# Performance work log

Hardware: AMD Instinct MI355X
Metric: run time of the kernel (lower is better)

## Reference

```python
import jax, jax.numpy as jnp
import numpy as np

B, S, D, E, H, K = 4, 2048, 1024, 8, 512, 2


def setup_inputs() -> dict:
    key = jax.random.key(0)
    ks = jax.random.split(key, 11)
    sc = 0.02
    return {
        "x": jax.random.normal(ks[0], (B, S, D), dtype=jnp.float32),
        "gate_W": jax.random.normal(ks[1], (D, E), dtype=jnp.float32) * sc,
        "W1": jax.random.normal(ks[2], (E, D, H), dtype=jnp.float32) * sc,
        "b1": jnp.zeros((E, H), dtype=jnp.float32),
        "W2": jax.random.normal(ks[3], (E, H, D), dtype=jnp.float32) * sc,
        "b2": jnp.zeros((E, D), dtype=jnp.float32),
        "Ws1": jax.random.normal(ks[4], (D, H), dtype=jnp.float32) * sc,
        "bs1": jnp.zeros((H,), dtype=jnp.float32),
        "Ws2": jax.random.normal(ks[5], (H, D), dtype=jnp.float32) * sc,
        "bs2": jnp.zeros((D,), dtype=jnp.float32),
        "route_scale": jnp.ones((), dtype=jnp.float32),
    }


def reference(x, gate_W, W1, b1, W2, b2, Ws1, bs1, Ws2, bs2, route_scale):
    # Gating: sigmoid scores scaled by route_scale (score_func='sigmoid')
    scores = jax.nn.sigmoid(x @ gate_W) * route_scale          # (B,S,E)
    topk_scores, topk_idx = jax.lax.top_k(scores, K)           # (B,S,K)
    topk_w = topk_scores / topk_scores.sum(-1, keepdims=True)  # normalized weights
    # Dense combine weights: zero for non-selected experts (same math as
    # the original sparse gather/scatter loop).
    onehot = jax.nn.one_hot(topk_idx, E, dtype=x.dtype)        # (B,S,K,E)
    gate_full = jnp.einsum('bsk,bske->bse', topk_w, onehot)    # (B,S,E)
    # Per-expert MLP applied to all tokens, combined with sparse gate weights.
    h = jax.nn.gelu(jnp.einsum('bsd,edh->bseh', x, W1) + b1, approximate=False)
    y = jnp.einsum('bseh,ehd->bsed', h, W2) + b2               # (B,S,E,D)
    expert_out = jnp.einsum('bse,bsed->bsd', gate_full, y)     # (B,S,D)
    # Shared expert MLP (always active)
    shared = jax.nn.gelu(x @ Ws1 + bs1, approximate=False) @ Ws2 + bs2
    return expert_out + shared
```

## Files before the change

### kernel.cpp

```cpp
#include <hip/hip_runtime.h>
#include <hip/hip_bf16.h>

#define TOKENS 8192
#define D_DIM  1024
#define E_NUM  8
#define H_DIM  512
#define N1     4608
#define CAP    3072
#define ET256  (CAP / 256)
#define EXP_ROWS (E_NUM * CAP)
#define SH_BASE  EXP_ROWS
#define HS_ROWS (EXP_ROWS + TOKENS)

typedef __bf16 bf16_t;
typedef __bf16 bf16x8 __attribute__((ext_vector_type(8)));
typedef __bf16 bf16x4 __attribute__((ext_vector_type(4)));
typedef float  f32x4  __attribute__((ext_vector_type(4)));

__device__ __forceinline__ float gelu_fast(float v) {
  float w = v * v;
  float t = __builtin_fmaf(w, 0.10294307f, 2.30258835f);
  float z = v * t;
  float e = __builtin_amdgcn_exp2f(z);
  float r = __builtin_amdgcn_rcpf(e + 1.0f);
  return v - v * r;
}

__global__ __launch_bounds__(256) void routing_kernel(
    const float* __restrict__ x, const float* __restrict__ gW,
    const float* __restrict__ route_scale, float* __restrict__ gateT,
    int* __restrict__ sel, bf16_t* __restrict__ Xb) {
  int tok  = blockIdx.x * 4 + (threadIdx.x >> 6);
  int lane = threadIdx.x & 63;
  const float* xr = x + (size_t)tok * D_DIM;
  double p[E_NUM];
#pragma unroll
  for (int e = 0; e < E_NUM; ++e) p[e] = 0.0;
  for (int d = lane; d < D_DIM; d += 64) {
    double xv = (double)xr[d];
    const float* g = gW + (size_t)d * E_NUM;
#pragma unroll
    for (int e = 0; e < E_NUM; ++e) p[e] += xv * (double)g[e];
  }
#pragma unroll
  for (int off = 32; off > 0; off >>= 1) {
#pragma unroll
    for (int e = 0; e < E_NUM; ++e) p[e] += __shfl_xor(p[e], off, 64);
  }
  if (lane == 0) {
    double rs = (double)route_scale[0];
    double s[E_NUM];
#pragma unroll
    for (int e = 0; e < E_NUM; ++e) s[e] = rs / (1.0 + exp(-p[e]));
    int i1 = 0;
#pragma unroll
    for (int e = 1; e < E_NUM; ++e) if (s[e] > s[i1]) i1 = e;
    int i2 = (i1 == 0) ? 1 : 0;
#pragma unroll
    for (int e = 0; e < E_NUM; ++e) if (e != i1 && s[e] > s[i2]) i2 = e;
    double inv = 1.0 / (s[i1] + s[i2]);
    float o[E_NUM];
#pragma unroll
    for (int e = 0; e < E_NUM; ++e) o[e] = 0.f;
    o[i1] = (float)(s[i1] * inv);
    o[i2] = (float)(s[i2] * inv);
#pragma unroll
    for (int e = 0; e < E_NUM; ++e) gateT[(size_t)e * TOKENS + tok] = o[e];
    sel[tok] = i1 * 8 + i2;
  }
  const float4* x4 = (const float4*)xr;
  bf16x4* xb4 = (bf16x4*)(Xb + (size_t)tok * D_DIM);
#pragma unroll
  for (int i = 0; i < 4; ++i) {
    float4 v = x4[i * 64 + lane];
    bf16x4 o = { (bf16_t)v.x, (bf16_t)v.y, (bf16_t)v.z, (bf16_t)v.w };
    xb4[i * 64 + lane] = o;
  }
}

__global__ __launch_bounds__(256) void repack1_kernel(
    const float* __restrict__ W1, const float* __restrict__ Ws1,
    bf16_t* __restrict__ Bt1) {
  __shared__ float tile[32][33];
  int k0 = blockIdx.x * 32, n0 = blockIdx.y * 32;
  int tx = threadIdx.x, ty = threadIdx.y;
#pragma unroll
  for (int i = 0; i < 4; ++i) {
    int kl = ty + i * 8;
    int n = n0 + tx, k = k0 + kl;
    float v;
    if (n0 < 4096) v = W1[(size_t)(n >> 9) * (D_DIM * H_DIM) + (size_t)k * H_DIM + (n & 511)];
    else           v = Ws1[(size_t)k * H_DIM + (n - 4096)];
    tile[kl][tx] = v;
  }
  __syncthreads();
#pragma unroll
  for (int i = 0; i < 4; ++i) {
    int nl = ty + i * 8;
    Bt1[(size_t)(n0 + nl) * D_DIM + k0 + tx] = (bf16_t)tile[tx][nl];
  }
}

__global__ __launch_bounds__(256) void repack2e_kernel(
    const float* __restrict__ W2, const float* __restrict__ Ws2,
    bf16_t* __restrict__ Bt2e) {
  __shared__ float tile[32][33];
  int d0 = blockIdx.x * 32, h0 = blockIdx.y * 32, e = blockIdx.z;
  int tx = threadIdx.x, ty = threadIdx.y;
#pragma unroll
  for (int i = 0; i < 4; ++i) {
    int hl = ty + i * 8;
    int h = h0 + hl, d = d0 + tx;
    float v = (e < E_NUM) ? W2[((size_t)e * H_DIM + h) * D_DIM + d]
                          : Ws2[(size_t)h * D_DIM + d];
    tile[hl][tx] = v;
  }
  __syncthreads();
#pragma unroll
  for (int i = 0; i < 4; ++i) {
    int dl = ty + i * 8;
    Bt2e[((size_t)e * D_DIM + (d0 + dl)) * H_DIM + h0 + tx] = (bf16_t)tile[tx][dl];
  }
}

__global__ __launch_bounds__(256) void listbuild_kernel(
    const float* __restrict__ gateT, const int* __restrict__ sel,
    int* __restrict__ perm, float* __restrict__ grow,
    int* __restrict__ tok2row, int* __restrict__ padcnt) {
  const int e = blockIdx.x;
  const int tid = threadIdx.x, lane = tid & 63, wid = tid >> 6;
  __shared__ int wsum[4];
  const float* row = gateT + (size_t)e * TOKENS;
  const int base = e * CAP;
  int running = 0;
  float gv = row[tid];
  for (int c = 0; c < TOKENS / 256; ++c) {
    float gv_next = (c + 1 < TOKENS / 256) ? row[(c + 1) * 256 + tid] : 0.f;
    const int tok = c * 256 + tid;
    const bool f = gv > 0.f;
    unsigned long long m = __ballot(f);
    int lanepre = __popcll(m & ((1ull << lane) - 1ull));
    if (lane == 0) wsum[wid] = __popcll(m);
    __syncthreads();
    int wbase = 0;
#pragma unroll
    for (int w2 = 0; w2 < 4; ++w2) if (w2 < wid) wbase += wsum[w2];
    const int tot = wsum[0] + wsum[1] + wsum[2] + wsum[3];
    if (f) {
      const int idx = running + wbase + lanepre;
      if (idx < CAP) {
        perm[base + idx] = tok;
        grow[base + idx] = gv;
        const int s = sel[tok];
        const int other = ((s >> 3) == e) ? (s & 7) : (s >> 3);
        tok2row[tok * 2 + (e > other ? 1 : 0)] = base + idx;
      }
    }
    running += tot;
    __syncthreads();
    gv = gv_next;
  }
  if (running > CAP) running = CAP;
  const int pc = (running + 255) & ~255;
  for (int i = running + tid; i < pc; i += 256) { perm[base + i] = 0; grow[base + i] = 0.f; }
  if (tid == 0) padcnt[e] = pc;
}

__device__ __forceinline__ void gload16(const char* src, char* dst) {
  __builtin_amdgcn_global_load_lds((const __attribute__((address_space(1))) void*)src,
      (__attribute__((address_space(3))) void*)dst, 16, 0, 0);
}

__device__ __forceinline__ void gemm_core256(
    const char* ga0, const char* ga1, const char* ga2, const char* ga3,
    const char* gb0, const char* gb1, const char* gb2, const char* gb3,
    int ktiles, char* lds, int wid, int lane, f32x4 (&acc)[8][4]) {
  const int wm = wid >> 2, wn = wid & 3;
  const int lA = lane & 15, kq = lane >> 4;
  const int slot0 = (kq ^ (lA & 7)) * 16;
  const int slot1 = ((4 + kq) ^ (lA & 7)) * 16;

  auto stage8 = [&](int buf, int t) {
    char* dA = lds + buf * 65536 + wid * 1024;
    char* dB = dA + 32768;
    const size_t ko = (size_t)t * 128;
    gload16(ga0 + ko, dA + 0 * 8192);
    gload16(ga1 + ko, dA + 1 * 8192);
    gload16(ga2 + ko, dA + 2 * 8192);
    gload16(ga3 + ko, dA + 3 * 8192);
    gload16(gb0 + ko, dB + 0 * 8192);
    gload16(gb1 + ko, dB + 1 * 8192);
    gload16(gb2 + ko, dB + 2 * 8192);
    gload16(gb3 + ko, dB + 3 * 8192);
  };

  stage8(0, 0);
  for (int t = 0; t < ktiles; ++t) {
    const int b = t & 1;
    if (t + 1 < ktiles) {
      stage8(b ^ 1, t + 1);
      asm volatile("s_waitcnt vmcnt(8)" ::: "memory");
    } else {
      asm volatile("s_waitcnt vmcnt(0)" ::: "memory");
    }
    __builtin_amdgcn_s_barrier();
    asm volatile("" ::: "memory");
    const char* Ab = lds + b * 65536 + wm * 16384;
    const char* Bb = lds + b * 65536 + 32768 + (wn >> 1) * 16384 + ((wn & 1) * 64) * 128;
    bf16x8 bfv[4][2];
#pragma unroll
    for (int nf = 0; nf < 4; ++nf) {
      const int rb = (nf * 16 + lA) * 128;
      bfv[nf][0] = *(const bf16x8*)(Bb + rb + slot0);
      bfv[nf][1] = *(const bf16x8*)(Bb + rb + slot1);
    }
#pragma unroll
    for (int qm = 0; qm < 2; ++qm) {
      bf16x8 af[4][2];
#pragma unroll
      for (int i = 0; i < 4; ++i) {
        const int ra = ((qm * 4 + i) * 16 + lA) * 128;
        af[i][0] = *(const bf16x8*)(Ab + ra + slot0);
        af[i][1] = *(const bf16x8*)(Ab + ra + slot1);
      }
      __builtin_amdgcn_s_setprio(1);
#pragma unroll
      for (int i = 0; i < 4; ++i)
#pragma unroll
        for (int nf = 0; nf < 4; ++nf) {
          acc[qm * 4 + i][nf] = __builtin_amdgcn_mfma_f32_16x16x32_bf16(af[i][0], bfv[nf][0], acc[qm * 4 + i][nf], 0, 0, 0);
          acc[qm * 4 + i][nf] = __builtin_amdgcn_mfma_f32_16x16x32_bf16(af[i][1], bfv[nf][1], acc[qm * 4 + i][nf], 0, 0, 0);
        }
      __builtin_amdgcn_s_setprio(0);
      __builtin_amdgcn_sched_barrier(0);
    }
    asm volatile("" ::: "memory");
    __builtin_amdgcn_s_barrier();
  }
}

__device__ __forceinline__ int swz_src(int lane) {
  return ((lane & 7) ^ ((lane >> 3) & 7)) * 16;
}

__global__ __launch_bounds__(512, 2) void gemm1e_kernel(
    const bf16_t* __restrict__ Xb, const bf16_t* __restrict__ Bt1,
    const int* __restrict__ perm, const float* __restrict__ grow,
    const int* __restrict__ padcnt,
    const float* __restrict__ b1, const float* __restrict__ bs1,
    bf16_t* __restrict__ Hs) {
  __shared__ bf16_t sL[65536];
  const int t = threadIdx.x, wid = t >> 6, lane = t & 63;
  const int L = blockIdx.x + 2 * blockIdx.y;
  const int xc = L & 7, ii = L >> 3;
  const int bx = xc >> 2;
  const int by = (xc & 3) * 32 + ii;
  int e, rowbase;
  if (by < E_NUM * ET256) {
    e = by / ET256;
    const int lt = by - e * ET256;
    if (lt * 256 >= padcnt[e]) return;
    rowbase = e * CAP + lt * 256;
  } else {
    e = E_NUM;
    rowbase = SH_BASE + (by - E_NUM * ET256) * 256;
  }
  const int n0 = bx * 256;
  const int rl = wid * 8 + (lane >> 3);
  const int sc = swz_src(lane);
  const char *ga[4], *gb[4];
#pragma unroll
  for (int g = 0; g < 4; ++g) {
    const int r = g * 64 + rl;
    const int tok = (e < E_NUM) ? perm[rowbase + r] : (rowbase - SH_BASE + r);
    ga[g] = (const char*)Xb + (size_t)tok * 2048 + sc;
    gb[g] = (const char*)(Bt1 + (size_t)e * H_DIM * D_DIM) + (size_t)(n0 + r) * 2048 + sc;
  }
  f32x4 acc[8][4];
#pragma unroll
  for (int i = 0; i < 8; ++i)
#pragma unroll
    for (int j = 0; j < 4; ++j) acc[i][j] = (f32x4){0.f, 0.f, 0.f, 0.f};
  gemm_core256(ga[0], ga[1], ga[2], ga[3], gb[0], gb[1], gb[2], gb[3],
               D_DIM / 64, (char*)sL, wid, lane, acc);

  const int wm = wid >> 2, wn = wid & 3, lA = lane & 15;
  const float* bias = (e < E_NUM) ? (b1 + e * H_DIM) : bs1;
#pragma unroll
  for (int mf = 0; mf < 8; ++mf) {
    const int rloc = wm * 128 + mf * 16 + (lane >> 4) * 4;
    float gr[4];
#pragma unroll
    for (int q = 0; q < 4; ++q)
      gr[q] = (e < E_NUM) ? grow[rowbase + rloc + q] : 1.0f;
#pragma unroll
    for (int nf = 0; nf < 4; ++nf) {
      const int col = n0 + wn * 64 + nf * 16 + lA;
      const float bv = bias[col];
#pragma unroll
      for (int q = 0; q < 4; ++q) {
        float v = gelu_fast(acc[mf][nf][q] + bv);
        Hs[(size_t)(rowbase + rloc + q) * H_DIM + col] = (bf16_t)(v * gr[q]);
      }
    }
  }
}

__global__ __launch_bounds__(512, 2) void gemm2e_kernel(
    const bf16_t* __restrict__ Hs, const bf16_t* __restrict__ Bt2e,
    const float* __restrict__ grow, const int* __restrict__ padcnt,
    const float* __restrict__ b2, bf16_t* __restrict__ Ys) {
  __shared__ bf16_t sL[65536];
  const int t = threadIdx.x, wid = t >> 6, lane = t & 63;
  const int L = blockIdx.x + 4 * blockIdx.y;
  const int xc = L & 7, ii = L >> 3;
  const int bx = xc >> 1;
  const int by = (xc & 1) * 48 + ii;
  const int e = by / ET256;
  const int lt = by - e * ET256;
  if (lt * 256 >= padcnt[e]) return;
  const int rowbase = e * CAP + lt * 256;
  const int n0 = bx * 256;
  const int rl = wid * 8 + (lane >> 3);
  const int sc = swz_src(lane);
  const char *ga[4], *gb[4];
#pragma unroll
  for (int g = 0; g < 4; ++g) {
    const int r = g * 64 + rl;
    ga[g] = (const char*)Hs + (size_t)(rowbase + r) * 1024 + sc;
    gb[g] = (const char*)(Bt2e + (size_t)e * D_DIM * H_DIM) + (size_t)(n0 + r) * 1024 + sc;
  }
  f32x4 acc[8][4];
#pragma unroll
  for (int i = 0; i < 8; ++i)
#pragma unroll
    for (int j = 0; j < 4; ++j) acc[i][j] = (f32x4){0.f, 0.f, 0.f, 0.f};
  gemm_core256(ga[0], ga[1], ga[2], ga[3], gb[0], gb[1], gb[2], gb[3],
               H_DIM / 64, (char*)sL, wid, lane, acc);

  const int wm = wid >> 2, wn = wid & 3, lA = lane & 15;
  const float* bb = b2 + (size_t)e * D_DIM;
#pragma unroll
  for (int mf = 0; mf < 8; ++mf) {
    const int rloc = wm * 128 + mf * 16 + (lane >> 4) * 4;
    float gr[4];
#pragma unroll
    for (int q = 0; q < 4; ++q) gr[q] = grow[rowbase + rloc + q];
#pragma unroll
    for (int nf = 0; nf < 4; ++nf) {
      const int col = n0 + wn * 64 + nf * 16 + lA;
      const float bv = bb[col];
#pragma unroll
      for (int q = 0; q < 4; ++q)
        Ys[(size_t)(rowbase + rloc + q) * D_DIM + col] = (bf16_t)(acc[mf][nf][q] + gr[q] * bv);
    }
  }
}

__global__ __launch_bounds__(512, 2) void gemm2s_kernel(
    const bf16_t* __restrict__ Hs, const bf16_t* __restrict__ Bt2e,
    const int* __restrict__ tok2row, const float* __restrict__ bs2,
    const bf16_t* __restrict__ Ys, float* __restrict__ out) {
  __shared__ bf16_t sL[65536];
  const int t = threadIdx.x, wid = t >> 6, lane = t & 63;
  const int L = blockIdx.x + 4 * blockIdx.y;
  const int xc = L & 7, ii = L >> 3;
  const int bx = xc >> 1;
  const int by = (xc & 1) * 16 + ii;
  const int tokbase = by * 256;
  const int rowbase = SH_BASE + tokbase;
  const int n0 = bx * 256;
  const int rl = wid * 8 + (lane >> 3);
  const int sc = swz_src(lane);
  const char *ga[4], *gb[4];
#pragma unroll
  for (int g = 0; g < 4; ++g) {
    const int r = g * 64 + rl;
    ga[g] = (const char*)Hs + (size_t)(rowbase + r) * 1024 + sc;
    gb[g] = (const char*)(Bt2e + (size_t)E_NUM * D_DIM * H_DIM) + (size_t)(n0 + r) * 1024 + sc;
  }
  f32x4 acc[8][4];
#pragma unroll
  for (int i = 0; i < 8; ++i)
#pragma unroll
    for (int j = 0; j < 4; ++j) acc[i][j] = (f32x4){0.f, 0.f, 0.f, 0.f};
  gemm_core256(ga[0], ga[1], ga[2], ga[3], gb[0], gb[1], gb[2], gb[3],
               H_DIM / 64, (char*)sL, wid, lane, acc);

  const int wm = wid >> 2, wn = wid & 3, lA = lane & 15;
#pragma unroll
  for (int mf = 0; mf < 8; ++mf) {
    const int rloc = wm * 128 + mf * 16 + (lane >> 4) * 4;
    int r0[4], r1[4];
#pragma unroll
    for (int q = 0; q < 4; ++q) {
      const int tok = tokbase + rloc + q;
      r0[q] = tok2row[tok * 2];
      r1[q] = tok2row[tok * 2 + 1];
    }
#pragma unroll
    for (int nf = 0; nf < 4; ++nf) {
      const int col = n0 + wn * 64 + nf * 16 + lA;
      const float bv = bs2[col];
#pragma unroll
      for (int q = 0; q < 4; ++q) {
        const int tok = tokbase + rloc + q;
        float y0 = (float)Ys[(size_t)r0[q] * D_DIM + col];
        float y1 = (float)Ys[(size_t)r1[q] * D_DIM + col];
        out[(size_t)tok * D_DIM + col] = acc[mf][nf][q] + bv + y0 + y1;
      }
    }
  }
}

extern "C" void kernel_launch(void* const* d_in, const int* in_sizes, int n_in,
                              void* d_out, int out_size, void* d_ws, size_t ws_size,
                              hipStream_t stream) {
  (void)in_sizes; (void)n_in; (void)out_size; (void)ws_size;
  const float* x    = (const float*)d_in[0];
  const float* gW   = (const float*)d_in[1];
  const float* W1   = (const float*)d_in[2];
  const float* b1   = (const float*)d_in[3];
  const float* W2   = (const float*)d_in[4];
  const float* b2   = (const float*)d_in[5];
  const float* Ws1  = (const float*)d_in[6];
  const float* bs1  = (const float*)d_in[7];
  const float* Ws2  = (const float*)d_in[8];
  const float* bs2  = (const float*)d_in[9];
  const float* rsc  = (const float*)d_in[10];
  float* out = (float*)d_out;

  char* w = (char*)d_ws;
  float*  gateT = (float*)w;  w += (size_t)E_NUM * TOKENS * 4;
  int*    sel   = (int*)w;    w += (size_t)TOKENS * 4;
  bf16_t* Xb    = (bf16_t*)w; w += (size_t)TOKENS * D_DIM * 2;
  bf16_t* Bt1   = (bf16_t*)w; w += (size_t)N1 * D_DIM * 2;
  bf16_t* Bt2e  = (bf16_t*)w; w += (size_t)9 * D_DIM * H_DIM * 2;
  bf16_t* Hs    = (bf16_t*)w; w += (size_t)HS_ROWS * H_DIM * 2;
  bf16_t* Ys    = (bf16_t*)w; w += (size_t)EXP_ROWS * D_DIM * 2;
  int*    perm  = (int*)w;    w += (size_t)EXP_ROWS * 4;
  float*  grow  = (float*)w;  w += (size_t)EXP_ROWS * 4;
  int*    tok2row = (int*)w;  w += (size_t)TOKENS * 2 * 4;
  int*    padcnt  = (int*)w;

  routing_kernel<<<TOKENS / 4, 256, 0, stream>>>(x, gW, rsc, gateT, sel, Xb);
  listbuild_kernel<<<E_NUM, 256, 0, stream>>>(gateT, sel, perm, grow, tok2row, padcnt);
  repack1_kernel<<<dim3(D_DIM / 32, N1 / 32), dim3(32, 8), 0, stream>>>(W1, Ws1, Bt1);
  repack2e_kernel<<<dim3(D_DIM / 32, H_DIM / 32, 9), dim3(32, 8), 0, stream>>>(W2, Ws2, Bt2e);

  gemm1e_kernel<<<dim3(H_DIM / 256, E_NUM * ET256 + TOKENS / 256), dim3(512), 0, stream>>>(
      Xb, Bt1, perm, grow, padcnt, b1, bs1, Hs);
  gemm2e_kernel<<<dim3(D_DIM / 256, E_NUM * ET256), dim3(512), 0, stream>>>(
      Hs, Bt2e, grow, padcnt, b2, Ys);
  gemm2s_kernel<<<dim3(D_DIM / 256, TOKENS / 256), dim3(512), 0, stream>>>(
      Hs, Bt2e, tok2row, bs2, Ys, out);
}
```

Measured before the change: 167.3 us.

## Merge weight repack kernels and restructure GEMM k-loop to single barrier

Fuses the two weight-repack launches into one kernel that dispatches on blockIdx.y, saving a launch. In the shared GEMM mainloop, the prefetch of the next k-tile now issues after a full vmcnt(0) wait and barrier, and the trailing barrier is dropped. Both LDS buffers stay in use, so the next load still overlaps with the MFMA work. The MFMA order is regrouped by k-half. The catch is that each iteration now waits for all outstanding loads before computing, which may expose memory latency that the old vmcnt(8) scheme hid.

After: 155.8 us. -6.8%, faster.

```diff
diff --git a/kernel.cpp b/kernel.cpp
--- a/kernel.cpp
+++ b/kernel.cpp
@@ -78,48 +78,48 @@
   }
 }
 
-__global__ __launch_bounds__(256) void repack1_kernel(
+__global__ __launch_bounds__(256) void repack_kernel(
     const float* __restrict__ W1, const float* __restrict__ Ws1,
-    bf16_t* __restrict__ Bt1) {
+    const float* __restrict__ W2, const float* __restrict__ Ws2,
+    bf16_t* __restrict__ Bt1, bf16_t* __restrict__ Bt2e) {
   __shared__ float tile[32][33];
-  int k0 = blockIdx.x * 32, n0 = blockIdx.y * 32;
-  int tx = threadIdx.x, ty = threadIdx.y;
-#pragma unroll
-  for (int i = 0; i < 4; ++i) {
-    int kl = ty + i * 8;
-    int n = n0 + tx, k = k0 + kl;
-    float v;
-    if (n0 < 4096) v = W1[(size_t)(n >> 9) * (D_DIM * H_DIM) + (size_t)k * H_DIM + (n & 511)];
-    else           v = Ws1[(size_t)k * H_DIM + (n - 4096)];
-    tile[kl][tx] = v;
-  }
-  __syncthreads();
-#pragma unroll
-  for (int i = 0; i < 4; ++i) {
-    int nl = ty + i * 8;
-    Bt1[(size_t)(n0 + nl) * D_DIM + k0 + tx] = (bf16_t)tile[tx][nl];
-  }
-}
-
-__global__ __launch_bounds__(256) void repack2e_kernel(
-    const float* __restrict__ W2, const float* __restrict__ Ws2,
-    bf16_t* __restrict__ Bt2e) {
-  __shared__ float tile[32][33];
-  int d0 = blockIdx.x * 32, h0 = blockIdx.y * 32, e = blockIdx.z;
-  int tx = threadIdx.x, ty = threadIdx.y;
-#pragma unroll
-  for (int i = 0; i < 4; ++i) {
-    int hl = ty + i * 8;
-    int h = h0 + hl, d = d0 + tx;
-    float v = (e < E_NUM) ? W2[((size_t)e * H_DIM + h) * D_DIM + d]
-                          : Ws2[(size_t)h * D_DIM + d];
-    tile[hl][tx] = v;
-  }
-  __syncthreads();
-#pragma unroll
-  for (int i = 0; i < 4; ++i) {
-    int dl = ty + i * 8;
-    Bt2e[((size_t)e * D_DIM + (d0 + dl)) * H_DIM + h0 + tx] = (bf16_t)tile[tx][dl];
+  const int tx = threadIdx.x, ty = threadIdx.y;
+  if (blockIdx.y < 144) {
+    const int k0 = blockIdx.x * 32, n0 = blockIdx.y * 32;
+#pragma unroll
+    for (int i = 0; i < 4; ++i) {
+      int kl = ty + i * 8;
+      int n = n0 + tx, k = k0 + kl;
+      float v;
+      if (n0 < 4096) v = W1[(size_t)(n >> 9) * (D_DIM * H_DIM) + (size_t)k * H_DIM + (n & 511)];
+      else           v = Ws1[(size_t)k * H_DIM + (n - 4096)];
+      tile[kl][tx] = v;
+    }
+    __syncthreads();
+#pragma unroll
+    for (int i = 0; i < 4; ++i) {
+      int nl = ty + i * 8;
+      Bt1[(size_t)(n0 + nl) * D_DIM + k0 + tx] = (bf16_t)tile[tx][nl];
+    }
+  } else {
+    const int yy = blockIdx.y - 144;
+    const int e = yy >> 4;
+    const int h0 = (yy & 15) * 32;
+    const int d0 = blockIdx.x * 32;
+#pragma unroll
+    for (int i = 0; i < 4; ++i) {
+      int hl = ty + i * 8;
+      int h = h0 + hl, d = d0 + tx;
+      float v = (e < E_NUM) ? W2[((size_t)e * H_DIM + h) * D_DIM + d]
+                            : Ws2[(size_t)h * D_DIM + d];
+      tile[hl][tx] = v;
+    }
+    __syncthreads();
+#pragma unroll
+    for (int i = 0; i < 4; ++i) {
+      int dl = ty + i * 8;
+      Bt2e[((size_t)e * D_DIM + (d0 + dl)) * H_DIM + h0 + tx] = (bf16_t)tile[tx][dl];
+    }
   }
 }
 
@@ -197,14 +197,10 @@
   stage8(0, 0);
   for (int t = 0; t < ktiles; ++t) {
     const int b = t & 1;
-    if (t + 1 < ktiles) {
-      stage8(b ^ 1, t + 1);
-      asm volatile("s_waitcnt vmcnt(8)" ::: "memory");
-    } else {
-      asm volatile("s_waitcnt vmcnt(0)" ::: "memory");
-    }
+    asm volatile("s_waitcnt vmcnt(0)" ::: "memory");
     __builtin_amdgcn_s_barrier();
     asm volatile("" ::: "memory");
+    if (t + 1 < ktiles) stage8(b ^ 1, t + 1);
     const char* Ab = lds + b * 65536 + wm * 16384;
     const char* Bb = lds + b * 65536 + 32768 + (wn >> 1) * 16384 + ((wn & 1) * 64) * 128;
     bf16x8 bfv[4][2];
@@ -225,17 +221,16 @@
       }
       __builtin_amdgcn_s_setprio(1);
 #pragma unroll
-      for (int i = 0; i < 4; ++i)
-#pragma unroll
-        for (int nf = 0; nf < 4; ++nf) {
-          acc[qm * 4 + i][nf] = __builtin_amdgcn_mfma_f32_16x16x32_bf16(af[i][0], bfv[nf][0], acc[qm * 4 + i][nf], 0, 0, 0);
-          acc[qm * 4 + i][nf] = __builtin_amdgcn_mfma_f32_16x16x32_bf16(af[i][1], bfv[nf][1], acc[qm * 4 + i][nf], 0, 0, 0);
-        }
+      for (int s = 0; s < 2; ++s)
+#pragma unroll
+        for (int i = 0; i < 4; ++i)
+#pragma unroll
+          for (int nf = 0; nf < 4; ++nf)
+            acc[qm * 4 + i][nf] = __builtin_amdgcn_mfma_f32_16x16x32_bf16(
+                af[i][s], bfv[nf][s], acc[qm * 4 + i][nf], 0, 0, 0);
       __builtin_amdgcn_s_setprio(0);
       __builtin_amdgcn_sched_barrier(0);
     }
-    asm volatile("" ::: "memory");
-    __builtin_amdgcn_s_barrier();
   }
 }
 
@@ -445,8 +440,7 @@
 
   routing_kernel<<<TOKENS / 4, 256, 0, stream>>>(x, gW, rsc, gateT, sel, Xb);
   listbuild_kernel<<<E_NUM, 256, 0, stream>>>(gateT, sel, perm, grow, tok2row, padcnt);
-  repack1_kernel<<<dim3(D_DIM / 32, N1 / 32), dim3(32, 8), 0, stream>>>(W1, Ws1, Bt1);
-  repack2e_kernel<<<dim3(D_DIM / 32, H_DIM / 32, 9), dim3(32, 8), 0, stream>>>(W2, Ws2, Bt2e);
+  repack_kernel<<<dim3(32, 288), dim3(32, 8), 0, stream>>>(W1, Ws1, W2, Ws2, Bt1, Bt2e);
 
   gemm1e_kernel<<<dim3(H_DIM / 256, E_NUM * ET256 + TOKENS / 256), dim3(512), 0, stream>>>(
       Xb, Bt1, perm, grow, padcnt, b1, bs1, Hs);
```
